# Optimization experiments

Hardware: AMD Instinct MI355X
Metric: run time of the kernel (lower is better)

## Reference

```python
import jax, jax.numpy as jnp
import numpy as np

N, M = 4096, 8192
IN_DIM, OUT_DIM = 4096, 1024
NUM_SAMPLE = 10


def setup_inputs() -> dict:
    key = jax.random.key(0)
    k1, k2, k3, k4, k5 = jax.random.split(key, 5)
    node_features = jax.random.normal(k1, (N, IN_DIM), dtype=jnp.float32)
    neighbor_features = jax.random.normal(k2, (M, IN_DIM), dtype=jnp.float32)
    # Xavier-ish scale for params
    weight = jax.random.normal(k3, (OUT_DIM, IN_DIM), dtype=jnp.float32) * (1.0 / np.sqrt(IN_DIM))
    attention_vector = jax.random.normal(k4, (2 * OUT_DIM, 1), dtype=jnp.float32) * 0.05
    neighbor_idx = jax.random.randint(k5, (N, NUM_SAMPLE), 0, M, dtype=jnp.int32)
    return {
        "node_features": node_features,
        "neighbor_features": neighbor_features,
        "weight": weight,
        "attention_vector": attention_vector,
        "neighbor_idx": neighbor_idx,
    }


def reference(node_features, neighbor_features, weight, attention_vector, neighbor_idx):
    # Linear transform: [N, out], [M, out]
    node_t = node_features @ weight.T
    neigh_t = neighbor_features @ weight.T

    # combined @ attention_vector decomposes:
    # cat([h_i, h_j]) @ a == h_i @ a1 + h_j @ a2  (same math, no [N,M,2*out] tensor)
    a1 = attention_vector[:OUT_DIM, 0]   # [out]
    a2 = attention_vector[OUT_DIM:, 0]   # [out]
    scores = jax.nn.leaky_relu((node_t @ a1)[:, None] + (neigh_t @ a2)[None, :],
                               negative_slope=0.2)  # [N, M]

    # Build dense 0/1 mask from sampled neighbor indices (ragged -> dense)
    rows = jnp.arange(N, dtype=jnp.int32)[:, None]                  # [N,1]
    mask = jnp.zeros((N, M), dtype=jnp.float32).at[rows, neighbor_idx].set(1.0)

    scores = jnp.where(mask == 0, -jnp.inf, scores)
    attn = jax.nn.softmax(scores, axis=1)           # masked softmax over neighbor pool
    return attn @ neigh_t                           # [N, out]
```

## Files before the change

kernel.cpp:

```cpp
#include <hip/hip_runtime.h>

#define IN_DIM  4096
#define OUT_DIM 1024
#define NN      4096
#define MM      8192
#define NSAMP   10

typedef __bf16 bf16x8 __attribute__((ext_vector_type(8)));
typedef float  fx4    __attribute__((ext_vector_type(4)));

__device__ __forceinline__ ushort f2bf(float f) {
    union { float f; unsigned u; } v; v.f = f;
    unsigned u = v.u;
    return (ushort)((u + 0x7FFFu + ((u >> 16) & 1u)) >> 16);
}
__device__ __forceinline__ float bf2f(ushort u) {
    union { unsigned u; float f; } v; v.u = ((unsigned)u) << 16;
    return v.f;
}

#define GLDS(g, l) __builtin_amdgcn_global_load_lds(                           \
    (const __attribute__((address_space(1))) unsigned*)(g),                    \
    (__attribute__((address_space(3))) unsigned*)(l), 16, 0, 0)

__global__ __launch_bounds__(256) void k_attvec(const float* __restrict__ W,
                                                const float* __restrict__ att,
                                                float* __restrict__ v1,
                                                float* __restrict__ v2,
                                                ushort* __restrict__ Wbf) {
    int k  = blockIdx.x * 256 + threadIdx.x;
    int o0 = blockIdx.y * 64;
    float s1 = 0.f, s2 = 0.f;
    for (int o = o0; o < o0 + 64; ++o) {
        float w = W[(size_t)o * IN_DIM + k];
        Wbf[(size_t)o * IN_DIM + k] = f2bf(w);
        s1 += att[o] * w;
        s2 += att[OUT_DIM + o] * w;
    }
    atomicAdd(&v1[k], s1);
    atomicAdd(&v2[k], s2);
}

__global__ __launch_bounds__(256) void k_rows(const float* __restrict__ node_f,
                                              const float* __restrict__ neigh_f,
                                              const float* __restrict__ v1,
                                              const float* __restrict__ v2,
                                              float* __restrict__ nalpha,
                                              float* __restrict__ nbeta,
                                              ushort* __restrict__ Abf) {
    int row = blockIdx.x;
    float s = 0.f;
    if (row < NN) {
        const float4* xr = reinterpret_cast<const float4*>(node_f + (size_t)row * IN_DIM);
        const float4* vr = reinterpret_cast<const float4*>(v1);
        for (int i = threadIdx.x; i < IN_DIM / 4; i += 256) {
            float4 a = xr[i], b = vr[i];
            s += a.x * b.x + a.y * b.y + a.z * b.z + a.w * b.w;
        }
    } else {
        int j = row - NN;
        const float4* xr = reinterpret_cast<const float4*>(neigh_f + (size_t)j * IN_DIM);
        const float4* vr = reinterpret_cast<const float4*>(v2);
        ushort4* yr = reinterpret_cast<ushort4*>(Abf + (size_t)j * IN_DIM);
        for (int i = threadIdx.x; i < IN_DIM / 4; i += 256) {
            float4 a = xr[i], b = vr[i];
            s += a.x * b.x + a.y * b.y + a.z * b.z + a.w * b.w;
            ushort4 o;
            o.x = f2bf(a.x); o.y = f2bf(a.y); o.z = f2bf(a.z); o.w = f2bf(a.w);
            yr[i] = o;
        }
    }
    for (int off = 32; off > 0; off >>= 1) s += __shfl_down(s, off, 64);
    __shared__ float ws[4];
    if ((threadIdx.x & 63) == 0) ws[threadIdx.x >> 6] = s;
    __syncthreads();
    if (threadIdx.x == 0) {
        float t = ws[0] + ws[1] + ws[2] + ws[3];
        if (row < NN) nalpha[row] = t; else nbeta[row - NN] = t;
    }
}

#define TM 128
#define TN 128
#define BK 32
#define KSPLIT (IN_DIM / 2)

__global__ __launch_bounds__(256, 4) void k_gemm(const ushort* __restrict__ A,
                                                 const ushort* __restrict__ B,
                                                 ushort* __restrict__ P) {
    __shared__ __align__(16) ushort As[TM * BK];
    __shared__ __align__(16) ushort Bs[TN * BK];
    const int tid  = threadIdx.x;
    const int lane = tid & 63;
    const int wave = tid >> 6;
    const int wm   = (wave >> 1) * 64;
    const int wn   = (wave & 1) * 64;
    const int bm   = blockIdx.x * TM;
    const int bn   = blockIdx.y * TN;
    const int kb   = blockIdx.z * KSPLIT;
    const int quad = lane >> 4;
    const int lrow = lane & 15;

    const int srow  = wave * 32 + (lane >> 2);
    const int skoff = (lane & 3) * 8;
    const ushort* gA = A + (size_t)(bm + srow) * IN_DIM + kb + skoff;
    const ushort* gB = B + (size_t)(bn + srow) * IN_DIM + kb + skoff;
    ushort* lA = As + wave * 1024;
    ushort* lB = Bs + wave * 1024;

    fx4 acc[4][4] = {};

    for (int k0 = 0; k0 < KSPLIT; k0 += BK) {
        GLDS(gA + k0,                lA);
        GLDS(gA + k0 + 16 * IN_DIM,  lA + 512);
        GLDS(gB + k0,                lB);
        GLDS(gB + k0 + 16 * IN_DIM,  lB + 512);
        __syncthreads();

        bf16x8 af[4], bfr[4];
#pragma unroll
        for (int mi = 0; mi < 4; ++mi)
            af[mi] = *reinterpret_cast<const bf16x8*>(As + (wm + mi * 16 + lrow) * BK + quad * 8);
#pragma unroll
        for (int ni = 0; ni < 4; ++ni)
            bfr[ni] = *reinterpret_cast<const bf16x8*>(Bs + (wn + ni * 16 + lrow) * BK + quad * 8);
#pragma unroll
        for (int mi = 0; mi < 4; ++mi)
#pragma unroll
            for (int ni = 0; ni < 4; ++ni)
                acc[mi][ni] = __builtin_amdgcn_mfma_f32_16x16x32_bf16(af[mi], bfr[ni], acc[mi][ni], 0, 0, 0);
        __syncthreads();
    }

    ushort* Pz = P + (size_t)blockIdx.z * MM * OUT_DIM;
#pragma unroll
    for (int mi = 0; mi < 4; ++mi)
#pragma unroll
        for (int ni = 0; ni < 4; ++ni) {
            int r = bm + wm + mi * 16 + quad * 4;
            int c = bn + wn + ni * 16 + lrow;
#pragma unroll
            for (int v = 0; v < 4; ++v)
                Pz[(size_t)(r + v) * OUT_DIM + c] = f2bf(acc[mi][ni][v]);
        }
}

__global__ __launch_bounds__(256) void k_aggregate(const ushort* __restrict__ P,
                                                   const float* __restrict__ nalpha,
                                                   const float* __restrict__ nbeta,
                                                   const int* __restrict__ nidx,
                                                   float* __restrict__ outp) {
    int row = blockIdx.x;
    __shared__ int   s_idx[NSAMP];
    __shared__ float s_w[NSAMP];
    if (threadIdx.x < 16) {
        int t = threadIdx.x;
        int j = (t < NSAMP) ? nidx[row * NSAMP + t] : -1;
        float score = -INFINITY;
        if (t < NSAMP) {
            float x = nalpha[row] + nbeta[j];
            score = x > 0.f ? x : 0.2f * x;
        }
        bool dup = false;
#pragma unroll
        for (int sIdx = 0; sIdx < NSAMP; ++sIdx) {
            int js = __shfl(j, sIdx, 16);
            if (sIdx < t && js == j) dup = true;
        }
        float mx = score;
#pragma unroll
        for (int off = 8; off > 0; off >>= 1) {
            float o = __shfl_xor(mx, off, 16);
            mx = o > mx ? o : mx;
        }
        float e = (t < NSAMP && !dup) ? expf(score - mx) : 0.f;
        float sum = e;
#pragma unroll
        for (int off = 8; off > 0; off >>= 1) sum += __shfl_xor(sum, off, 16);
        if (t < NSAMP) {
            s_idx[t] = j;
            s_w[t]   = e / sum;
        }
    }
    __syncthreads();
    int col = threadIdx.x * 4;
    float ax = 0.f, ay = 0.f, az = 0.f, aw = 0.f;
#pragma unroll
    for (int t = 0; t < NSAMP; ++t) {
        float w = s_w[t];
        size_t off = (size_t)s_idx[t] * OUT_DIM + col;
        ushort4 u0 = *reinterpret_cast<const ushort4*>(P + off);
        ushort4 u1 = *reinterpret_cast<const ushort4*>(P + (size_t)MM * OUT_DIM + off);
        ax += w * (bf2f(u0.x) + bf2f(u1.x));
        ay += w * (bf2f(u0.y) + bf2f(u1.y));
        az += w * (bf2f(u0.z) + bf2f(u1.z));
        aw += w * (bf2f(u0.w) + bf2f(u1.w));
    }
    float4 o; o.x = ax; o.y = ay; o.z = az; o.w = aw;
    *reinterpret_cast<float4*>(outp + (size_t)row * OUT_DIM + col) = o;
}

extern "C" void kernel_launch(void* const* d_in, const int* in_sizes, int n_in,
                              void* d_out, int out_size, void* d_ws, size_t ws_size,
                              hipStream_t stream) {
    const float* node_f  = (const float*)d_in[0];
    const float* neigh_f = (const float*)d_in[1];
    const float* W       = (const float*)d_in[2];
    const float* att     = (const float*)d_in[3];
    const int*   nidx    = (const int*)d_in[4];
    float* outp = (float*)d_out;

    char* ws = (char*)d_ws;
    ushort* Abf = (ushort*)ws;
    ushort* Wbf = (ushort*)(ws + 67108864);
    ushort* P   = (ushort*)(ws + 75497472);
    float*  v1     = (float*)(ws + 109051904);
    float*  v2     = v1 + IN_DIM;
    float*  nalpha = v2 + IN_DIM;
    float*  nbeta  = nalpha + NN;

    hipMemsetAsync(v1, 0, 2 * IN_DIM * sizeof(float), stream);

    k_attvec   <<<dim3(16, 16), 256, 0, stream>>>(W, att, v1, v2, Wbf);
    k_rows     <<<NN + MM,      256, 0, stream>>>(node_f, neigh_f, v1, v2, nalpha, nbeta, Abf);
    k_gemm     <<<dim3(MM / TM, OUT_DIM / TN, 2), 256, 0, stream>>>(Abf, Wbf, P);
    k_aggregate<<<NN,           256, 0, stream>>>(P, nalpha, nbeta, nidx, outp);
}
```

Baseline: 379.9 us.

## Rewrite GEMM with 256x256 tiles, 4-stage LDS pipeline, swizzle; retune prep kernels

The bf16 GEMM now uses 512-thread blocks computing 256x256 tiles. It loads through a 4-deep LDS ring buffer with partial vmcnt waits, so global loads overlap MFMA work, and uses an XOR-swizzled LDS layout to avoid bank conflicts. A block-id remap improves L2 locality, and s_setprio raises priority around the MFMA bursts. The row-dot kernel now assigns one row per wave with no shared-memory reduction, and the attvec kernel is split into more blocks. The larger tiles and buffers raise register and LDS pressure, and the grid shrinks to 256 blocks.

```diff
diff --git a/kernel.cpp b/kernel.cpp
--- a/kernel.cpp
+++ b/kernel.cpp
@@ -29,9 +29,9 @@
                                                 float* __restrict__ v2,
                                                 ushort* __restrict__ Wbf) {
     int k  = blockIdx.x * 256 + threadIdx.x;
-    int o0 = blockIdx.y * 64;
+    int o0 = blockIdx.y * 32;
     float s1 = 0.f, s2 = 0.f;
-    for (int o = o0; o < o0 + 64; ++o) {
+    for (int o = o0; o < o0 + 32; ++o) {
         float w = W[(size_t)o * IN_DIM + k];
         Wbf[(size_t)o * IN_DIM + k] = f2bf(w);
         s1 += att[o] * w;
@@ -48,12 +48,14 @@
                                               float* __restrict__ nalpha,
                                               float* __restrict__ nbeta,
                                               ushort* __restrict__ Abf) {
-    int row = blockIdx.x;
+    int row  = blockIdx.x * 4 + (threadIdx.x >> 6);
+    int lane = threadIdx.x & 63;
     float s = 0.f;
     if (row < NN) {
         const float4* xr = reinterpret_cast<const float4*>(node_f + (size_t)row * IN_DIM);
         const float4* vr = reinterpret_cast<const float4*>(v1);
-        for (int i = threadIdx.x; i < IN_DIM / 4; i += 256) {
+#pragma unroll
+        for (int i = lane; i < IN_DIM / 4; i += 64) {
             float4 a = xr[i], b = vr[i];
             s += a.x * b.x + a.y * b.y + a.z * b.z + a.w * b.w;
         }
@@ -62,7 +64,8 @@
         const float4* xr = reinterpret_cast<const float4*>(neigh_f + (size_t)j * IN_DIM);
         const float4* vr = reinterpret_cast<const float4*>(v2);
         ushort4* yr = reinterpret_cast<ushort4*>(Abf + (size_t)j * IN_DIM);
-        for (int i = threadIdx.x; i < IN_DIM / 4; i += 256) {
+#pragma unroll
+        for (int i = lane; i < IN_DIM / 4; i += 64) {
             float4 a = xr[i], b = vr[i];
             s += a.x * b.x + a.y * b.y + a.z * b.z + a.w * b.w;
             ushort4 o;
@@ -70,75 +73,109 @@
             yr[i] = o;
         }
     }
+#pragma unroll
     for (int off = 32; off > 0; off >>= 1) s += __shfl_down(s, off, 64);
-    __shared__ float ws[4];
-    if ((threadIdx.x & 63) == 0) ws[threadIdx.x >> 6] = s;
-    __syncthreads();
-    if (threadIdx.x == 0) {
-        float t = ws[0] + ws[1] + ws[2] + ws[3];
-        if (row < NN) nalpha[row] = t; else nbeta[row - NN] = t;
-    }
-}
-
-#define TM 128
-#define TN 128
-#define BK 32
+    if (lane == 0) {
+        if (row < NN) nalpha[row] = s; else nbeta[row - NN] = s;
+    }
+}
+
+#define BMT 256
+#define BNT 256
+#define BKG 32
 #define KSPLIT (IN_DIM / 2)
-
-__global__ __launch_bounds__(256, 4) void k_gemm(const ushort* __restrict__ A,
+#define NT (KSPLIT / BKG)
+
+__device__ __forceinline__ void tile_compute(const ushort* __restrict__ as,
+                                             const ushort* __restrict__ bs,
+                                             int aoff, int boff,
+                                             fx4 (&acc)[8][4]) {
+    bf16x8 af[8], bfr[4];
+#pragma unroll
+    for (int mi = 0; mi < 8; ++mi)
+        af[mi] = *reinterpret_cast<const bf16x8*>(as + aoff + mi * 512);
+#pragma unroll
+    for (int ni = 0; ni < 4; ++ni)
+        bfr[ni] = *reinterpret_cast<const bf16x8*>(bs + boff + ni * 512);
+    __builtin_amdgcn_s_setprio(1);
+#pragma unroll
+    for (int mi = 0; mi < 8; ++mi)
+#pragma unroll
+        for (int ni = 0; ni < 4; ++ni)
+            acc[mi][ni] = __builtin_amdgcn_mfma_f32_16x16x32_bf16(af[mi], bfr[ni], acc[mi][ni], 0, 0, 0);
+    __builtin_amdgcn_s_setprio(0);
+}
+
+__global__ __launch_bounds__(512, 2) void k_gemm(const ushort* __restrict__ A,
                                                  const ushort* __restrict__ B,
                                                  ushort* __restrict__ P) {
-    __shared__ __align__(16) ushort As[TM * BK];
-    __shared__ __align__(16) ushort Bs[TN * BK];
+    __shared__ __align__(16) ushort As[4][BMT * BKG];
+    __shared__ __align__(16) ushort Bs[4][BNT * BKG];
+
     const int tid  = threadIdx.x;
     const int lane = tid & 63;
-    const int wave = tid >> 6;
-    const int wm   = (wave >> 1) * 64;
-    const int wn   = (wave & 1) * 64;
-    const int bm   = blockIdx.x * TM;
-    const int bn   = blockIdx.y * TN;
-    const int kb   = blockIdx.z * KSPLIT;
-    const int quad = lane >> 4;
+    const int wid  = tid >> 6;
+    const int wr   = wid >> 2;
+    const int wc   = wid & 3;
     const int lrow = lane & 15;
-
-    const int srow  = wave * 32 + (lane >> 2);
-    const int skoff = (lane & 3) * 8;
-    const ushort* gA = A + (size_t)(bm + srow) * IN_DIM + kb + skoff;
-    const ushort* gB = B + (size_t)(bn + srow) * IN_DIM + kb + skoff;
-    ushort* lA = As + wave * 1024;
-    ushort* lB = Bs + wave * 1024;
-
-    fx4 acc[4][4] = {};
-
-    for (int k0 = 0; k0 < KSPLIT; k0 += BK) {
-        GLDS(gA + k0,                lA);
-        GLDS(gA + k0 + 16 * IN_DIM,  lA + 512);
-        GLDS(gB + k0,                lB);
-        GLDS(gB + k0 + 16 * IN_DIM,  lB + 512);
-        __syncthreads();
-
-        bf16x8 af[4], bfr[4];
-#pragma unroll
-        for (int mi = 0; mi < 4; ++mi)
-            af[mi] = *reinterpret_cast<const bf16x8*>(As + (wm + mi * 16 + lrow) * BK + quad * 8);
-#pragma unroll
-        for (int ni = 0; ni < 4; ++ni)
-            bfr[ni] = *reinterpret_cast<const bf16x8*>(Bs + (wn + ni * 16 + lrow) * BK + quad * 8);
-#pragma unroll
-        for (int mi = 0; mi < 4; ++mi)
-#pragma unroll
-            for (int ni = 0; ni < 4; ++ni)
-                acc[mi][ni] = __builtin_amdgcn_mfma_f32_16x16x32_bf16(af[mi], bfr[ni], acc[mi][ni], 0, 0, 0);
-        __syncthreads();
-    }
-
-    ushort* Pz = P + (size_t)blockIdx.z * MM * OUT_DIM;
-#pragma unroll
-    for (int mi = 0; mi < 4; ++mi)
+    const int q    = lane >> 4;
+
+    const int bid = blockIdx.x;
+    const int swz = (bid & 7) * 32 + (bid >> 3);
+    const int tx  = swz & 31;
+    const int ty  = (swz >> 5) & 3;
+    const int tz  = swz >> 7;
+    const int bm  = tx * BMT;
+    const int bn  = ty * BNT;
+    const int kb  = tz * KSPLIT;
+
+    const int sr  = tid >> 2;
+    const int scu = (((tid & 3) ^ (sr & 3)) << 3);
+    const ushort* gA0 = A + (size_t)(bm + sr) * IN_DIM + kb + scu;
+    const ushort* gA1 = gA0 + (size_t)128 * IN_DIM;
+    const ushort* gB0 = B + (size_t)(bn + sr) * IN_DIM + kb + scu;
+    const ushort* gB1 = gB0 + (size_t)128 * IN_DIM;
+    const int wbase = wid * 512;
+
+#define STAGE(buf, kt) do {                                                    \
+        GLDS(gA0 + (size_t)(kt) * BKG, &As[buf][0]        + wbase);            \
+        GLDS(gA1 + (size_t)(kt) * BKG, &As[buf][0] + 4096 + wbase);            \
+        GLDS(gB0 + (size_t)(kt) * BKG, &Bs[buf][0]        + wbase);            \
+        GLDS(gB1 + (size_t)(kt) * BKG, &Bs[buf][0] + 4096 + wbase);            \
+    } while (0)
+
+    const int qs   = ((q ^ (lrow & 3)) << 3);
+    const int aoff = (wr * 128 + lrow) * BKG + qs;
+    const int boff = (wc * 64  + lrow) * BKG + qs;
+
+    fx4 acc[8][4] = {};
+
+    STAGE(0, 0); STAGE(1, 1); STAGE(2, 2);
+    asm volatile("s_waitcnt vmcnt(8)" ::: "memory");
+    __builtin_amdgcn_s_barrier();
+
+    for (int t = 0; t < NT - 3; ++t) {
+        STAGE((t + 3) & 3, t + 3);
+        tile_compute(&As[t & 3][0], &Bs[t & 3][0], aoff, boff, acc);
+        asm volatile("s_waitcnt vmcnt(8)" ::: "memory");
+        __builtin_amdgcn_s_barrier();
+    }
+    tile_compute(&As[(NT - 3) & 3][0], &Bs[(NT - 3) & 3][0], aoff, boff, acc);
+    asm volatile("s_waitcnt vmcnt(4)" ::: "memory");
+    __builtin_amdgcn_s_barrier();
+    tile_compute(&As[(NT - 2) & 3][0], &Bs[(NT - 2) & 3][0], aoff, boff, acc);
+    asm volatile("s_waitcnt vmcnt(0)" ::: "memory");
+    __builtin_amdgcn_s_barrier();
+    tile_compute(&As[(NT - 1) & 3][0], &Bs[(NT - 1) & 3][0], aoff, boff, acc);
+#undef STAGE
+
+    ushort* Pz = P + (size_t)tz * MM * OUT_DIM;
+#pragma unroll
+    for (int mi = 0; mi < 8; ++mi)
 #pragma unroll
         for (int ni = 0; ni < 4; ++ni) {
-            int r = bm + wm + mi * 16 + quad * 4;
-            int c = bn + wn + ni * 16 + lrow;
+            int r = bm + wr * 128 + mi * 16 + q * 4;
+            int c = bn + wc * 64  + ni * 16 + lrow;
 #pragma unroll
             for (int v = 0; v < 4; ++v)
                 Pz[(size_t)(r + v) * OUT_DIM + c] = f2bf(acc[mi][ni][v]);
@@ -221,8 +258,8 @@
 
     hipMemsetAsync(v1, 0, 2 * IN_DIM * sizeof(float), stream);
 
-    k_attvec   <<<dim3(16, 16), 256, 0, stream>>>(W, att, v1, v2, Wbf);
-    k_rows     <<<NN + MM,      256, 0, stream>>>(node_f, neigh_f, v1, v2, nalpha, nbeta, Abf);
-    k_gemm     <<<dim3(MM / TM, OUT_DIM / TN, 2), 256, 0, stream>>>(Abf, Wbf, P);
-    k_aggregate<<<NN,           256, 0, stream>>>(P, nalpha, nbeta, nidx, outp);
-}
+    k_attvec   <<<dim3(16, 32),   256, 0, stream>>>(W, att, v1, v2, Wbf);
+    k_rows     <<<(NN + MM) / 4,  256, 0, stream>>>(node_f, neigh_f, v1, v2, nalpha, nbeta, Abf);
+    k_gemm     <<<256,            512, 0, stream>>>(Abf, Wbf, P);
+    k_aggregate<<<NN,             256, 0, stream>>>(P, nalpha, nbeta, nidx, outp);
+}
```

Result: slower. 410.0 us (+7.9%).
